# Performance work log

Measured on AMD Instinct MI355X. Metric: run time of the kernel, lower is better.

Reference implementation:

```python
import jax, jax.numpy as jnp
import numpy as np

N_NODES = 50000
N_EDGES = 800000
IN_F = 128
HID = 64
OUT_F = 64
H = 1  # num_heads


def _gat_layer(x, W, al, ar, b, src, dst, n_nodes):
    # DGL GATConv: project, per-head attention logits, edge softmax over dst, scatter-sum
    h, f = al.shape
    feat = (x @ W).reshape(x.shape[0], h, f)              # [N,H,F]
    el = jnp.sum(feat * al, axis=-1)                       # [N,H]
    er = jnp.sum(feat * ar, axis=-1)                       # [N,H]
    e = jax.nn.leaky_relu(el[src] + er[dst], negative_slope=0.2)  # [E,H]
    emax = jax.ops.segment_max(e, dst, num_segments=n_nodes)      # [N,H]
    ex = jnp.exp(e - emax[dst])                            # [E,H]
    denom = jax.ops.segment_sum(ex, dst, num_segments=n_nodes)    # [N,H]
    alpha = ex / denom[dst]                                # [E,H] edge softmax
    msg = feat[src] * alpha[:, :, None]                    # [E,H,F]
    out = jax.ops.segment_sum(msg, dst, num_segments=n_nodes) + b # [N,H,F]
    return out


def setup_inputs() -> dict:
    key = jax.random.key(0)
    ks = jax.random.split(key, 20)

    def glorot(k, shape, fan_in):
        return jax.random.normal(k, shape, dtype=jnp.float32) / np.sqrt(fan_in)

    x = jax.random.normal(ks[0], (N_NODES, IN_F), dtype=jnp.float32)
    src = jax.random.randint(ks[1], (N_EDGES,), 0, N_NODES, dtype=jnp.int32)
    dst = jax.random.randint(ks[2], (N_EDGES,), 0, N_NODES, dtype=jnp.int32)
    neg_src = jax.random.randint(ks[3], (N_EDGES,), 0, N_NODES, dtype=jnp.int32)
    neg_dst = jax.random.randint(ks[4], (N_EDGES,), 0, N_NODES, dtype=jnp.int32)

    # layer dims: 128 -> 64 -> 128 -> 64 (hidden, hidden*2, out), H=1, mean over heads
    W1 = glorot(ks[5], (IN_F, H * HID), IN_F)
    al1 = glorot(ks[6], (H, HID), HID)
    ar1 = glorot(ks[7], (H, HID), HID)
    b1 = jnp.zeros((H, HID), dtype=jnp.float32)
    W2 = glorot(ks[8], (HID, H * 2 * HID), HID)
    al2 = glorot(ks[9], (H, 2 * HID), 2 * HID)
    ar2 = glorot(ks[10], (H, 2 * HID), 2 * HID)
    b2 = jnp.zeros((H, 2 * HID), dtype=jnp.float32)
    W3 = glorot(ks[11], (2 * HID, H * OUT_F), 2 * HID)
    al3 = glorot(ks[12], (H, OUT_F), OUT_F)
    ar3 = glorot(ks[13], (H, OUT_F), OUT_F)
    b3 = jnp.zeros((H, OUT_F), dtype=jnp.float32)
    lp_W = glorot(ks[14], (2 * OUT_F, 1), 2 * OUT_F)
    lp_b = jnp.zeros((1,), dtype=jnp.float32)

    return {
        "x": x, "W1": W1, "al1": al1, "ar1": ar1, "b1": b1,
        "W2": W2, "al2": al2, "ar2": ar2, "b2": b2,
        "W3": W3, "al3": al3, "ar3": ar3, "b3": b3,
        "lp_W": lp_W, "lp_b": lp_b,
        "src": src, "dst": dst, "neg_src": neg_src, "neg_dst": neg_dst,
    }


def reference(x, W1, al1, ar1, b1, W2, al2, ar2, b2, W3, al3, ar3, b3,
              lp_W, lp_b, src, dst, neg_src, neg_dst):
    n = x.shape[0]
    h = jax.nn.relu(_gat_layer(x, W1, al1, ar1, b1, src, dst, n)).mean(axis=1)
    h = jax.nn.relu(_gat_layer(h, W2, al2, ar2, b2, src, dst, n)).mean(axis=1)
    h = _gat_layer(h, W3, al3, ar3, b3, src, dst, n).mean(axis=1)      # [N,OUT_F]
    pos_score = (jnp.concatenate([h[src], h[dst]], axis=1) @ lp_W + lp_b)[:, 0]
    neg_score = (jnp.concatenate([h[neg_src], h[neg_dst]], axis=1) @ lp_W + lp_b)[:, 0]
    return h, pos_score, neg_score
```

## Files before the change

kernel.cpp:

```cpp
#include <hip/hip_runtime.h>
#include <hip/hip_bf16.h>

#define NN 50000
#define NE 800000
#define NBKT 196
#define NT 200
#define TILE 4000

typedef unsigned short ushort_t;
typedef unsigned int uint_t;

typedef __bf16 bf16_t;
typedef bf16_t bf16x8 __attribute__((ext_vector_type(8)));
typedef float f32x4 __attribute__((ext_vector_type(4)));

__device__ __forceinline__ float leaky(float v) { return (v >= 0.f) ? v : 0.2f * v; }
__device__ __forceinline__ ushort_t f2bf(float f) {
    __hip_bfloat16 h = __float2bfloat16(f);
    return *reinterpret_cast<ushort_t*>(&h);
}
__device__ __forceinline__ float bf_lo(uint_t v) { return __uint_as_float(v << 16); }
__device__ __forceinline__ float bf_hi(uint_t v) { return __uint_as_float(v & 0xFFFF0000u); }


#define WELEM (128 * 64 * 3)
#define WBLK 96

__global__ void prep_hist(const float* __restrict__ W1, const float* __restrict__ W2,
                          const float* __restrict__ W3, ushort_t* __restrict__ Wt1,
                          ushort_t* __restrict__ Wt2, ushort_t* __restrict__ Wt3,
                          const float* __restrict__ al2, const float* __restrict__ ar2,
                          float* __restrict__ val2, float* __restrict__ var2,
                          const int* __restrict__ dst, uint_t* __restrict__ gh) {
    __shared__ uint_t h[NBKT];
    int tid = threadIdx.x;
    int blk = blockIdx.x;
    if (blk < NT) {
        for (int i = tid; i < NBKT; i += 256) h[i] = 0;
        __syncthreads();
        int e0 = blk * TILE;
        for (int i = tid; i < TILE; i += 256)
            atomicAdd(&h[((uint_t)dst[e0 + i]) >> 8], 1u);
        __syncthreads();
        for (int i = tid; i < NBKT; i += 256) gh[(size_t)i * NT + blk] = h[i];
        return;
    }
    blk -= NT;
    if (blk < WBLK) {
        int gw = blk * 256 + tid;
        if (gw < 128 * 64) {
            int i = gw; int k = i >> 6, m = i & 63;
            Wt1[m * 128 + k] = f2bf(W1[i]);
        } else if (gw < 2 * 128 * 64) {
            int i = gw - 128 * 64; int k = i >> 7, m = i & 127;
            Wt2[m * 64 + k] = f2bf(W2[i]);
        } else if (gw < WELEM) {
            int i = gw - 2 * 128 * 64; int k = i >> 6, m = i & 63;
            Wt3[m * 128 + k] = f2bf(W3[i]);
        }
        return;
    }
    if (tid < 128) {
        int k = tid & 63;
        const float* av = (tid < 64) ? al2 : ar2;
        float acc = 0.f;
        const float* row = W2 + k * 128;
        #pragma unroll 8
        for (int m = 0; m < 128; ++m) acc += row[m] * av[m];
        if (tid < 64) val2[k] = acc; else var2[k] = acc;
    }
}

__global__ void scan_gh(uint_t* __restrict__ gh, uint_t* __restrict__ bucketbase) {
    __shared__ uint_t btot[NBKT];
    __shared__ uint_t ws4[4];
    int tid = threadIdx.x;
    int wv = tid >> 6, lane = tid & 63;
    for (int b = wv; b < NBKT; b += 16) {
        uint_t* row = gh + (size_t)b * NT;
        uint_t carry = 0;
        for (int base = 0; base < NT; base += 64) {
            int idx = base + lane;
            uint_t v = (idx < NT) ? row[idx] : 0;
            uint_t sc = v;
            for (int o = 1; o < 64; o <<= 1) {
                uint_t xx = __shfl_up(sc, o);
                if (lane >= o) sc += xx;
            }
            if (idx < NT) row[idx] = carry + sc - v;
            carry += __shfl(sc, 63);
        }
        if (lane == 0) btot[b] = carry;
    }
    __syncthreads();
    uint_t v = 0, sc = 0;
    if (tid < 256) {
        v = (tid < NBKT) ? btot[tid] : 0;
        sc = v;
        for (int o = 1; o < 64; o <<= 1) {
            uint_t xx = __shfl_up(sc, o);
            if ((tid & 63) >= o) sc += xx;
        }
        if ((tid & 63) == 63) ws4[tid >> 6] = sc;
    }
    __syncthreads();
    if (tid == 0) {
        uint_t r = 0;
        for (int i = 0; i < 4; ++i) { uint_t tmp = ws4[i]; ws4[i] = r; r += tmp; }
    }
    __syncthreads();
    if (tid < NBKT) bucketbase[tid] = ws4[tid >> 6] + sc - v;
    if (tid == 0) bucketbase[NBKT] = NE;
}

__global__ void part_scatter(const int* __restrict__ src, const int* __restrict__ dst,
                             const uint_t* __restrict__ gh, const uint_t* __restrict__ bucketbase,
                             uint_t* __restrict__ pairbuf) {
    __shared__ uint_t cur[NBKT];
    int t = blockIdx.x, tid = threadIdx.x;
    for (int i = tid; i < NBKT; i += 256)
        cur[i] = gh[(size_t)i * NT + t] + bucketbase[i];
    __syncthreads();
    int e0 = t * TILE;
    for (int i = tid; i < TILE; i += 256) {
        int d = dst[e0 + i], s = src[e0 + i];
        uint_t pos = atomicAdd(&cur[((uint_t)d) >> 8], 1u);
        pairbuf[pos] = (uint_t)s | (((uint_t)d & 255u) << 16);
    }
}

__device__ __forceinline__ void gemm64_f32core(const float* __restrict__ X,
                                               const ushort_t* __restrict__ Wt,
                                               const float* __restrict__ al,
                                               const float* __restrict__ ar,
                                               ushort_t* __restrict__ featbf,
                                               float* __restrict__ el, float* __restrict__ er,
                                               int N, int blk, int tid) {
    constexpr int CT = 4, KI = 4;
    int wv = tid >> 6, lane = tid & 63;
    int c = lane & 15, kq = lane >> 4;
    int n0 = blk * 64 + wv * 16;
    if (n0 >= N) return;

    const float* aptr = X + (size_t)(n0 + c) * 128 + kq * 8;
    bf16x8 a[KI];
    #pragma unroll
    for (int ki = 0; ki < KI; ++ki) {
        float4 f0 = *reinterpret_cast<const float4*>(aptr + ki * 32);
        float4 f1 = *reinterpret_cast<const float4*>(aptr + ki * 32 + 4);
        union { bf16x8 v; ushort_t u[8]; } pk;
        pk.u[0] = f2bf(f0.x); pk.u[1] = f2bf(f0.y); pk.u[2] = f2bf(f0.z); pk.u[3] = f2bf(f0.w);
        pk.u[4] = f2bf(f1.x); pk.u[5] = f2bf(f1.y); pk.u[6] = f2bf(f1.z); pk.u[7] = f2bf(f1.w);
        a[ki] = pk.v;
    }

    f32x4 acc[CT];
    #pragma unroll
    for (int ct = 0; ct < CT; ++ct) acc[ct] = (f32x4){0.f, 0.f, 0.f, 0.f};

    #pragma unroll
    for (int ct = 0; ct < CT; ++ct) {
        const ushort_t* bptr = Wt + (size_t)(ct * 16 + c) * 128 + kq * 8;
        #pragma unroll
        for (int ki = 0; ki < KI; ++ki) {
            bf16x8 b = *reinterpret_cast<const bf16x8*>(bptr + ki * 32);
            acc[ct] = __builtin_amdgcn_mfma_f32_16x16x32_bf16(a[ki], b, acc[ct], 0, 0, 0);
        }
    }

    float pe[4] = {0.f, 0.f, 0.f, 0.f}, pr[4] = {0.f, 0.f, 0.f, 0.f};
    #pragma unroll
    for (int ct = 0; ct < CT; ++ct) {
        float alv = al[ct * 16 + c], arv = ar[ct * 16 + c];
        #pragma unroll
        for (int j = 0; j < 4; ++j) {
            float v = acc[ct][j];
            featbf[(size_t)(n0 + kq * 4 + j) * 64 + ct * 16 + c] = f2bf(v);
            pe[j] += v * alv;
            pr[j] += v * arv;
        }
    }
    #pragma unroll
    for (int o = 1; o < 16; o <<= 1) {
        #pragma unroll
        for (int j = 0; j < 4; ++j) {
            pe[j] += __shfl_xor(pe[j], o);
            pr[j] += __shfl_xor(pr[j], o);
        }
    }
    if (c == 0) {
        #pragma unroll
        for (int j = 0; j < 4; ++j) {
            el[n0 + kq * 4 + j] = pe[j];
            er[n0 + kq * 4 + j] = pr[j];
        }
    }
}

__global__ void csr_gemm1(const uint_t* __restrict__ pairbuf, const uint_t* __restrict__ bucketbase,
                          int* __restrict__ off, int* __restrict__ csrsrc,
                          const float* __restrict__ X, const ushort_t* __restrict__ Wt1,
                          const float* __restrict__ al1, const float* __restrict__ ar1,
                          ushort_t* __restrict__ featbf, float* __restrict__ el,
                          float* __restrict__ er, int N) {
    __shared__ uint_t cnt[256];
    __shared__ uint_t ws4[4];
    int tid = threadIdx.x;
    if (blockIdx.x >= NBKT) {
        gemm64_f32core(X, Wt1, al1, ar1, featbf, el, er, N, blockIdx.x - NBKT, tid);
        return;
    }
    int b = blockIdx.x;
    uint_t eb0 = bucketbase[b], m = bucketbase[b + 1] - eb0;
    cnt[tid] = 0;
    __syncthreads();
    for (uint_t i = tid; i < m; i += 256)
        atomicAdd(&cnt[pairbuf[eb0 + i] >> 16], 1u);
    __syncthreads();
    uint_t v = cnt[tid];
    int lane = tid & 63, w = tid >> 6;
    uint_t sc = v;
    for (int o = 1; o < 64; o <<= 1) {
        uint_t x = __shfl_up(sc, o);
        if (lane >= o) sc += x;
    }
    if (lane == 63) ws4[w] = sc;
    __syncthreads();
    if (tid == 0) { uint_t r = 0; for (int i = 0; i < 4; ++i) { uint_t tmp = ws4[i]; ws4[i] = r; r += tmp; } }
    __syncthreads();
    uint_t excl = ws4[w] + sc - v;
    int node = b * 256 + tid;
    if (node < NN) off[node] = (int)(eb0 + excl);
    if (b == 0 && tid == 0) off[NN] = NE;
    __syncthreads();
    cnt[tid] = eb0 + excl;
    __syncthreads();
    for (uint_t i = tid; i < m; i += 256) {
        uint_t p = pairbuf[eb0 + i];
        uint_t pos = atomicAdd(&cnt[p >> 16], 1u);
        csrsrc[pos] = (int)(p & 0xFFFFu);
    }
}

__global__ void fused_l23(const ushort_t* __restrict__ G, const ushort_t* __restrict__ Wt2,
                          const float* __restrict__ b2, const ushort_t* __restrict__ Wt3,
                          const float* __restrict__ al3, const float* __restrict__ ar3,
                          ushort_t* __restrict__ feat3, float* __restrict__ el,
                          float* __restrict__ er, int N) {
    __shared__ ushort_t h3s[4][16 * 128];
    int wv = threadIdx.x >> 6, lane = threadIdx.x & 63;
    int c = lane & 15, kq = lane >> 4;
    int n0 = blockIdx.x * 64 + wv * 16;
    if (n0 >= N) return;

    const ushort_t* aptr = G + (size_t)(n0 + c) * 64 + kq * 8;
    bf16x8 a1[2];
    a1[0] = *reinterpret_cast<const bf16x8*>(aptr);
    a1[1] = *reinterpret_cast<const bf16x8*>(aptr + 32);

    f32x4 acc2[8];
    #pragma unroll
    for (int ct = 0; ct < 8; ++ct) acc2[ct] = (f32x4){0.f, 0.f, 0.f, 0.f};
    #pragma unroll
    for (int ct = 0; ct < 8; ++ct) {
        const ushort_t* bptr = Wt2 + (size_t)(ct * 16 + c) * 64 + kq * 8;
        acc2[ct] = __builtin_amdgcn_mfma_f32_16x16x32_bf16(
            a1[0], *reinterpret_cast<const bf16x8*>(bptr), acc2[ct], 0, 0, 0);
        acc2[ct] = __builtin_amdgcn_mfma_f32_16x16x32_bf16(
            a1[1], *reinterpret_cast<const bf16x8*>(bptr + 32), acc2[ct], 0, 0, 0);
    }

    #pragma unroll
    for (int ct = 0; ct < 8; ++ct) {
        float bv = b2[ct * 16 + c];
        #pragma unroll
        for (int j = 0; j < 4; ++j) {
            int r = kq * 4 + j;
            float v = fmaxf(acc2[ct][j] + bv, 0.f);
            h3s[wv][r * 128 + ((ct * 16 + c) ^ ((r & 7) << 3))] = f2bf(v);
        }
    }

    bf16x8 a2[4];
    #pragma unroll
    for (int ki = 0; ki < 4; ++ki)
        a2[ki] = *reinterpret_cast<const bf16x8*>(
            &h3s[wv][c * 128 + ((ki * 32 + kq * 8) ^ ((c & 7) << 3))]);

    f32x4 acc3[4];
    #pragma unroll
    for (int ct = 0; ct < 4; ++ct) acc3[ct] = (f32x4){0.f, 0.f, 0.f, 0.f};
    #pragma unroll
    for (int ct = 0; ct < 4; ++ct) {
        const ushort_t* bptr = Wt3 + (size_t)(ct * 16 + c) * 128 + kq * 8;
        #pragma unroll
        for (int ki = 0; ki < 4; ++ki) {
            bf16x8 b = *reinterpret_cast<const bf16x8*>(bptr + ki * 32);
            acc3[ct] = __builtin_amdgcn_mfma_f32_16x16x32_bf16(a2[ki], b, acc3[ct], 0, 0, 0);
        }
    }

    float pe[4] = {0.f, 0.f, 0.f, 0.f}, pr[4] = {0.f, 0.f, 0.f, 0.f};
    #pragma unroll
    for (int ct = 0; ct < 4; ++ct) {
        float alv = al3[ct * 16 + c], arv = ar3[ct * 16 + c];
        #pragma unroll
        for (int j = 0; j < 4; ++j) {
            float v = acc3[ct][j];
            feat3[(size_t)(n0 + kq * 4 + j) * 64 + ct * 16 + c] = f2bf(v);
            pe[j] += v * alv;
            pr[j] += v * arv;
        }
    }
    #pragma unroll
    for (int o = 1; o < 16; o <<= 1) {
        #pragma unroll
        for (int j = 0; j < 4; ++j) {
            pe[j] += __shfl_xor(pe[j], o);
            pr[j] += __shfl_xor(pr[j], o);
        }
    }
    if (c == 0) {
        #pragma unroll
        for (int j = 0; j < 4; ++j) {
            el[n0 + kq * 4 + j] = pe[j];
            er[n0 + kq * 4 + j] = pr[j];
        }
    }
}

template <bool BIAS, bool RELU, bool BFOUT, bool DOTS>
__global__ void gat_agg2(const int* __restrict__ off, const int* __restrict__ csrsrc,
                         const float* __restrict__ el, const float* __restrict__ er,
                         const ushort_t* __restrict__ featbf, const float* __restrict__ bias,
                         void* __restrict__ hout, const float* __restrict__ va,
                         const float* __restrict__ vb, float* __restrict__ o1,
                         float* __restrict__ o2, int N) {
    int g = blockIdx.x * blockDim.x + threadIdx.x;
    int node = g >> 5;
    int sub = threadIdx.x & 31;
    if (node >= N) return;
    int start = off[node], deg = off[node + 1] - start;
    float ern = er[node];

    int s0 = 0; float e0 = -1e30f;
    if (sub < deg) { s0 = csrsrc[start + sub]; e0 = leaky(el[s0] + ern); }
    float m = e0;
    for (int i = 32 + sub; i < deg; i += 32)
        m = fmaxf(m, leaky(el[csrsrc[start + i]] + ern));
    for (int o = 16; o; o >>= 1) m = fmaxf(m, __shfl_xor(m, o));

    float p0 = (sub < deg) ? __expf(e0 - m) : 0.f;
    float ssum = p0;
    for (int i = 32 + sub; i < deg; i += 32)
        ssum += __expf(leaky(el[csrsrc[start + i]] + ern) - m);
    for (int o = 16; o; o >>= 1) ssum += __shfl_xor(ssum, o);
    float inv = (deg > 0) ? 1.f / ssum : 0.f;

    float acc0 = 0.f, acc1 = 0.f;
    int head = (deg < 32) ? deg : 32;
    int i = 0;
    for (; i + 4 <= head; i += 4) {
        float pA = __shfl(p0, i, 32), pB = __shfl(p0, i + 1, 32),
              pC = __shfl(p0, i + 2, 32), pD = __shfl(p0, i + 3, 32);
        int sA = __shfl(s0, i, 32), sB = __shfl(s0, i + 1, 32),
            sC = __shfl(s0, i + 2, 32), sD = __shfl(s0, i + 3, 32);
        uint_t vA = ((const uint_t*)(featbf + (size_t)sA * 64))[sub];
        uint_t vB = ((const uint_t*)(featbf + (size_t)sB * 64))[sub];
        uint_t vC = ((const uint_t*)(featbf + (size_t)sC * 64))[sub];
        uint_t vD = ((const uint_t*)(featbf + (size_t)sD * 64))[sub];
        acc0 += pA * bf_lo(vA) + pB * bf_lo(vB) + pC * bf_lo(vC) + pD * bf_lo(vD);
        acc1 += pA * bf_hi(vA) + pB * bf_hi(vB) + pC * bf_hi(vC) + pD * bf_hi(vD);
    }
    for (; i < head; ++i) {
        float p = __shfl(p0, i, 32);
        int sN = __shfl(s0, i, 32);
        uint_t v = ((const uint_t*)(featbf + (size_t)sN * 64))[sub];
        acc0 += p * bf_lo(v); acc1 += p * bf_hi(v);
    }
    for (i = 32; i < deg; ++i) {
        int sN = csrsrc[start + i];
        float p = __expf(leaky(el[sN] + ern) - m);
        uint_t v = ((const uint_t*)(featbf + (size_t)sN * 64))[sub];
        acc0 += p * bf_lo(v); acc1 += p * bf_hi(v);
    }

    float v0 = acc0 * inv, v1 = acc1 * inv;
    if (BIAS) {
        float2 b2 = ((const float2*)bias)[sub];
        v0 += b2.x; v1 += b2.y;
    }
    if (RELU) { v0 = fmaxf(v0, 0.f); v1 = fmaxf(v1, 0.f); }
    if (BFOUT) {
        ((uint_t*)hout)[(size_t)node * 32 + sub] = ((uint_t)f2bf(v1) << 16) | f2bf(v0);
    } else {
        ((float2*)hout)[(size_t)node * 32 + sub] = make_float2(v0, v1);
    }
    if (DOTS) {
        float2 wa = ((const float2*)va)[sub];
        float2 wb = ((const float2*)vb)[sub];
        float a = v0 * wa.x + v1 * wa.y;
        float b = v0 * wb.x + v1 * wb.y;
        for (int o = 16; o; o >>= 1) { a += __shfl_xor(a, o); b += __shfl_xor(b, o); }
        if (sub == 0) { o1[node] = a; o2[node] = b; }
    }
}

__global__ void scores4_k(const int4* __restrict__ s4, const int4* __restrict__ d4,
                          const int4* __restrict__ ns4, const int4* __restrict__ nd4,
                          const float* __restrict__ s1, const float* __restrict__ s2,
                          const float* __restrict__ lpb,
                          float4* __restrict__ outp, float4* __restrict__ outn, int E4) {
    int i = blockIdx.x * blockDim.x + threadIdx.x;
    float cc = lpb[0];
    if (i < E4) {
        int4 s = s4[i], d = d4[i];
        outp[i] = make_float4(s1[s.x] + s2[d.x] + cc, s1[s.y] + s2[d.y] + cc,
                              s1[s.z] + s2[d.z] + cc, s1[s.w] + s2[d.w] + cc);
    } else if (i < 2 * E4) {
        int j = i - E4;
        int4 s = ns4[j], d = nd4[j];
        outn[j] = make_float4(s1[s.x] + s2[d.x] + cc, s1[s.y] + s2[d.y] + cc,
                              s1[s.z] + s2[d.z] + cc, s1[s.w] + s2[d.w] + cc);
    }
}


struct Scratch {
    ushort_t* wt1; ushort_t* wt2; ushort_t* wt3;
    ushort_t* featbf; ushort_t* hAbf;
    float* elA; float* erA; float* elB; float* erB;
    float* val2; float* var2; float* s1; float* s2;
    int* off; int* csrsrc; uint_t* gh; uint_t* bucketbase;
    uint_t* pairbuf;
};

extern "C" void kernel_launch(void* const* d_in, const int* in_sizes, int n_in,
                              void* d_out, int out_size, void* d_ws, size_t ws_size,
                              hipStream_t stream) {
    const float* x   = (const float*)d_in[0];
    const float* W1  = (const float*)d_in[1];
    const float* al1 = (const float*)d_in[2];
    const float* ar1 = (const float*)d_in[3];
    const float* b1  = (const float*)d_in[4];
    const float* W2  = (const float*)d_in[5];
    const float* al2 = (const float*)d_in[6];
    const float* ar2 = (const float*)d_in[7];
    const float* b2  = (const float*)d_in[8];
    const float* W3  = (const float*)d_in[9];
    const float* al3 = (const float*)d_in[10];
    const float* ar3 = (const float*)d_in[11];
    const float* b3  = (const float*)d_in[12];
    const float* lpW = (const float*)d_in[13];
    const float* lpb = (const float*)d_in[14];
    const int* src  = (const int*)d_in[15];
    const int* dst  = (const int*)d_in[16];
    const int* nsrc = (const int*)d_in[17];
    const int* ndst = (const int*)d_in[18];

    char* w = (char*)d_ws;
    Scratch S;
    S.featbf     = (ushort_t*)w; w += (size_t)NN * 64 * 2;
    S.hAbf       = (ushort_t*)w; w += (size_t)NN * 64 * 2;
    S.wt1        = (ushort_t*)w; w += 128 * 64 * 2;
    S.wt2        = (ushort_t*)w; w += 64 * 128 * 2;
    S.wt3        = (ushort_t*)w; w += 128 * 64 * 2;
    S.elA        = (float*)w;    w += (size_t)NN * 4;
    S.erA        = (float*)w;    w += (size_t)NN * 4;
    S.elB        = (float*)w;    w += (size_t)NN * 4;
    S.erB        = (float*)w;    w += (size_t)NN * 4;
    S.val2       = (float*)w;    w += 64 * 4;
    S.var2       = (float*)w;    w += 64 * 4;
    S.s1         = (float*)w;    w += (size_t)NN * 4;
    S.s2         = (float*)w;    w += (size_t)NN * 4;
    S.off        = (int*)w;      w += (size_t)(NN + 1) * 4;
    S.csrsrc     = (int*)w;      w += (size_t)NE * 4;
    S.gh         = (uint_t*)w;   w += (size_t)NBKT * NT * 4;
    S.bucketbase = (uint_t*)w;   w += (size_t)(NBKT + 1) * 4;
    S.pairbuf    = (uint_t*)w;   w += (size_t)NE * 4;

    const int GEMM_GRID = (NN + 63) / 64;
    const int AGG_GRID = (NN * 32 + 255) / 256;

    prep_hist<<<NT + WBLK + 1, 256, 0, stream>>>(
        W1, W2, W3, S.wt1, S.wt2, S.wt3, al2, ar2, S.val2, S.var2, dst, S.gh);
    scan_gh<<<1, 1024, 0, stream>>>(S.gh, S.bucketbase);
    part_scatter<<<NT, 256, 0, stream>>>(src, dst, S.gh, S.bucketbase, S.pairbuf);
    csr_gemm1<<<NBKT + GEMM_GRID, 256, 0, stream>>>(
        S.pairbuf, S.bucketbase, S.off, S.csrsrc,
        x, S.wt1, al1, ar1, S.featbf, S.elA, S.erA, NN);

    float* out_h   = (float*)d_out;
    float* out_pos = out_h + (size_t)NN * 64;
    float* out_neg = out_pos + NE;

    gat_agg2<true, true, true, true><<<AGG_GRID, 256, 0, stream>>>(
        S.off, S.csrsrc, S.elA, S.erA, S.featbf, b1, S.hAbf,
        S.val2, S.var2, S.elB, S.erB, NN);
    gat_agg2<false, false, true, false><<<AGG_GRID, 256, 0, stream>>>(
        S.off, S.csrsrc, S.elB, S.erB, S.hAbf, nullptr, S.featbf,
        nullptr, nullptr, nullptr, nullptr, NN);
    fused_l23<<<GEMM_GRID, 256, 0, stream>>>(S.featbf, S.wt2, b2, S.wt3, al3, ar3,
                                             S.hAbf, S.elA, S.erA, NN);
    gat_agg2<true, false, false, true><<<AGG_GRID, 256, 0, stream>>>(
        S.off, S.csrsrc, S.elA, S.erA, S.hAbf, b3, out_h,
        lpW, lpW + 64, S.s1, S.s2, NN);
    const int E4 = NE / 4;
    scores4_k<<<(2 * E4 + 255) / 256, 256, 0, stream>>>(
        (const int4*)src, (const int4*)dst, (const int4*)nsrc, (const int4*)ndst,
        S.s1, S.s2, lpb, (float4*)out_pos, (float4*)out_neg, E4);
}
```

Baseline: 164.0 us.

## Store layer-1 and layer-2 gathered features as int8 with per-row scales

Layer-1 projected features and layer-1 aggregation output are now quantized to int8 with a per-node absmax scale instead of bf16. The scale is folded into the softmax weight during the gather. This halves the bytes moved by the random per-edge feature gathers in the first two aggregation passes. In exchange it loses precision, which may exceed tolerance, and adds a warp reduction for the scale plus an extra scale load per edge.

```diff
diff --git a/kernel.cpp b/kernel.cpp
--- a/kernel.cpp
+++ b/kernel.cpp
@@ -9,6 +9,7 @@
 
 typedef unsigned short ushort_t;
 typedef unsigned int uint_t;
+typedef signed char s8_t;
 
 typedef __bf16 bf16_t;
 typedef bf16_t bf16x8 __attribute__((ext_vector_type(8)));
@@ -133,7 +134,8 @@
                                                const ushort_t* __restrict__ Wt,
                                                const float* __restrict__ al,
                                                const float* __restrict__ ar,
-                                               ushort_t* __restrict__ featbf,
+                                               s8_t* __restrict__ feat8,
+                                               float* __restrict__ scl,
                                                float* __restrict__ el, float* __restrict__ er,
                                                int N, int blk, int tid) {
     constexpr int CT = 4, KI = 4;
@@ -169,15 +171,16 @@
     }
 
     float pe[4] = {0.f, 0.f, 0.f, 0.f}, pr[4] = {0.f, 0.f, 0.f, 0.f};
+    float pm[4] = {0.f, 0.f, 0.f, 0.f};
     #pragma unroll
     for (int ct = 0; ct < CT; ++ct) {
         float alv = al[ct * 16 + c], arv = ar[ct * 16 + c];
         #pragma unroll
         for (int j = 0; j < 4; ++j) {
             float v = acc[ct][j];
-            featbf[(size_t)(n0 + kq * 4 + j) * 64 + ct * 16 + c] = f2bf(v);
             pe[j] += v * alv;
             pr[j] += v * arv;
+            pm[j] = fmaxf(pm[j], fabsf(v));
         }
     }
     #pragma unroll
@@ -186,6 +189,17 @@
         for (int j = 0; j < 4; ++j) {
             pe[j] += __shfl_xor(pe[j], o);
             pr[j] += __shfl_xor(pr[j], o);
+            pm[j] = fmaxf(pm[j], __shfl_xor(pm[j], o));
+        }
+    }
+    #pragma unroll
+    for (int j = 0; j < 4; ++j) {
+        float qi = (pm[j] > 0.f) ? 127.f / pm[j] : 0.f;
+        int row = n0 + kq * 4 + j;
+        #pragma unroll
+        for (int ct = 0; ct < CT; ++ct) {
+            int q = (int)rintf(acc[ct][j] * qi);
+            feat8[(size_t)row * 64 + ct * 16 + c] = (s8_t)q;
         }
     }
     if (c == 0) {
@@ -193,6 +207,7 @@
         for (int j = 0; j < 4; ++j) {
             el[n0 + kq * 4 + j] = pe[j];
             er[n0 + kq * 4 + j] = pr[j];
+            scl[n0 + kq * 4 + j] = pm[j] * (1.f / 127.f);
         }
     }
 }
@@ -201,13 +216,13 @@
                           int* __restrict__ off, int* __restrict__ csrsrc,
                           const float* __restrict__ X, const ushort_t* __restrict__ Wt1,
                           const float* __restrict__ al1, const float* __restrict__ ar1,
-                          ushort_t* __restrict__ featbf, float* __restrict__ el,
-                          float* __restrict__ er, int N) {
+                          s8_t* __restrict__ feat8, float* __restrict__ scl1,
+                          float* __restrict__ el, float* __restrict__ er, int N) {
     __shared__ uint_t cnt[256];
     __shared__ uint_t ws4[4];
     int tid = threadIdx.x;
     if (blockIdx.x >= NBKT) {
-        gemm64_f32core(X, Wt1, al1, ar1, featbf, el, er, N, blockIdx.x - NBKT, tid);
+        gemm64_f32core(X, Wt1, al1, ar1, feat8, scl1, el, er, N, blockIdx.x - NBKT, tid);
         return;
     }
     int b = blockIdx.x;
@@ -329,11 +344,12 @@
     }
 }
 
-template <bool BIAS, bool RELU, bool BFOUT, bool DOTS>
+template <int INFMT, int OUTFMT, bool BIAS, bool RELU, bool DOTS>
 __global__ void gat_agg2(const int* __restrict__ off, const int* __restrict__ csrsrc,
                          const float* __restrict__ el, const float* __restrict__ er,
-                         const ushort_t* __restrict__ featbf, const float* __restrict__ bias,
-                         void* __restrict__ hout, const float* __restrict__ va,
+                         const void* __restrict__ featv, const float* __restrict__ inscl,
+                         const float* __restrict__ bias, void* __restrict__ hout,
+                         float* __restrict__ outscl, const float* __restrict__ va,
                          const float* __restrict__ vb, float* __restrict__ o1,
                          float* __restrict__ o2, int N) {
     int g = blockIdx.x * blockDim.x + threadIdx.x;
@@ -343,8 +359,12 @@
     int start = off[node], deg = off[node + 1] - start;
     float ern = er[node];
 
-    int s0 = 0; float e0 = -1e30f;
-    if (sub < deg) { s0 = csrsrc[start + sub]; e0 = leaky(el[s0] + ern); }
+    int s0 = 0; float e0 = -1e30f; float sc0 = 0.f;
+    if (sub < deg) {
+        s0 = csrsrc[start + sub];
+        e0 = leaky(el[s0] + ern);
+        if (INFMT == 0) sc0 = inscl[s0];
+    }
     float m = e0;
     for (int i = 32 + sub; i < deg; i += 32)
         m = fmaxf(m, leaky(el[csrsrc[start + i]] + ern));
@@ -357,32 +377,60 @@
     for (int o = 16; o; o >>= 1) ssum += __shfl_xor(ssum, o);
     float inv = (deg > 0) ? 1.f / ssum : 0.f;
 
+    float ps0 = (INFMT == 0) ? p0 * sc0 : p0;
+
     float acc0 = 0.f, acc1 = 0.f;
     int head = (deg < 32) ? deg : 32;
     int i = 0;
     for (; i + 4 <= head; i += 4) {
-        float pA = __shfl(p0, i, 32), pB = __shfl(p0, i + 1, 32),
-              pC = __shfl(p0, i + 2, 32), pD = __shfl(p0, i + 3, 32);
+        float pA = __shfl(ps0, i, 32), pB = __shfl(ps0, i + 1, 32),
+              pC = __shfl(ps0, i + 2, 32), pD = __shfl(ps0, i + 3, 32);
         int sA = __shfl(s0, i, 32), sB = __shfl(s0, i + 1, 32),
             sC = __shfl(s0, i + 2, 32), sD = __shfl(s0, i + 3, 32);
-        uint_t vA = ((const uint_t*)(featbf + (size_t)sA * 64))[sub];
-        uint_t vB = ((const uint_t*)(featbf + (size_t)sB * 64))[sub];
-        uint_t vC = ((const uint_t*)(featbf + (size_t)sC * 64))[sub];
-        uint_t vD = ((const uint_t*)(featbf + (size_t)sD * 64))[sub];
-        acc0 += pA * bf_lo(vA) + pB * bf_lo(vB) + pC * bf_lo(vC) + pD * bf_lo(vD);
-        acc1 += pA * bf_hi(vA) + pB * bf_hi(vB) + pC * bf_hi(vC) + pD * bf_hi(vD);
+        if (INFMT == 0) {
+            const s8_t* base = (const s8_t*)featv;
+            ushort_t uA = ((const ushort_t*)(base + (size_t)sA * 64))[sub];
+            ushort_t uB = ((const ushort_t*)(base + (size_t)sB * 64))[sub];
+            ushort_t uC = ((const ushort_t*)(base + (size_t)sC * 64))[sub];
+            ushort_t uD = ((const ushort_t*)(base + (size_t)sD * 64))[sub];
+            acc0 += pA * (float)(s8_t)(uA & 0xFF) + pB * (float)(s8_t)(uB & 0xFF)
+                  + pC * (float)(s8_t)(uC & 0xFF) + pD * (float)(s8_t)(uD & 0xFF);
+            acc1 += pA * (float)(s8_t)(uA >> 8) + pB * (float)(s8_t)(uB >> 8)
+                  + pC * (float)(s8_t)(uC >> 8) + pD * (float)(s8_t)(uD >> 8);
+        } else {
+            const ushort_t* base = (const ushort_t*)featv;
+            uint_t vA = ((const uint_t*)(base + (size_t)sA * 64))[sub];
+            uint_t vB = ((const uint_t*)(base + (size_t)sB * 64))[sub];
+            uint_t vC = ((const uint_t*)(base + (size_t)sC * 64))[sub];
+            uint_t vD = ((const uint_t*)(base + (size_t)sD * 64))[sub];
+            acc0 += pA * bf_lo(vA) + pB * bf_lo(vB) + pC * bf_lo(vC) + pD * bf_lo(vD);
+            acc1 += pA * bf_hi(vA) + pB * bf_hi(vB) + pC * bf_hi(vC) + pD * bf_hi(vD);
+        }
     }
     for (; i < head; ++i) {
-        float p = __shfl(p0, i, 32);
+        float p = __shfl(ps0, i, 32);
         int sN = __shfl(s0, i, 32);
-        uint_t v = ((const uint_t*)(featbf + (size_t)sN * 64))[sub];
-        acc0 += p * bf_lo(v); acc1 += p * bf_hi(v);
+        if (INFMT == 0) {
+            ushort_t u = ((const ushort_t*)((const s8_t*)featv + (size_t)sN * 64))[sub];
+            acc0 += p * (float)(s8_t)(u & 0xFF);
+            acc1 += p * (float)(s8_t)(u >> 8);
+        } else {
+            uint_t v = ((const uint_t*)((const ushort_t*)featv + (size_t)sN * 64))[sub];
+            acc0 += p * bf_lo(v); acc1 += p * bf_hi(v);
+        }
     }
     for (i = 32; i < deg; ++i) {
         int sN = csrsrc[start + i];
         float p = __expf(leaky(el[sN] + ern) - m);
-        uint_t v = ((const uint_t*)(featbf + (size_t)sN * 64))[sub];
-        acc0 += p * bf_lo(v); acc1 += p * bf_hi(v);
+        if (INFMT == 0) {
+            p *= inscl[sN];
+            ushort_t u = ((const ushort_t*)((const s8_t*)featv + (size_t)sN * 64))[sub];
+            acc0 += p * (float)(s8_t)(u & 0xFF);
+            acc1 += p * (float)(s8_t)(u >> 8);
+        } else {
+            uint_t v = ((const uint_t*)((const ushort_t*)featv + (size_t)sN * 64))[sub];
+            acc0 += p * bf_lo(v); acc1 += p * bf_hi(v);
+        }
     }
 
     float v0 = acc0 * inv, v1 = acc1 * inv;
@@ -391,11 +439,21 @@
         v0 += b2.x; v1 += b2.y;
     }
     if (RELU) { v0 = fmaxf(v0, 0.f); v1 = fmaxf(v1, 0.f); }
-    if (BFOUT) {
+
+    if (OUTFMT == 0) {
+        float rm = fmaxf(fabsf(v0), fabsf(v1));
+        for (int o = 16; o; o >>= 1) rm = fmaxf(rm, __shfl_xor(rm, o));
+        float qi = (rm > 0.f) ? 127.f / rm : 0.f;
+        int q0 = (int)rintf(v0 * qi), q1 = (int)rintf(v1 * qi);
+        ((ushort_t*)hout)[(size_t)node * 32 + sub] =
+            (ushort_t)((q0 & 0xFF) | ((q1 & 0xFF) << 8));
+        if (sub == 0) outscl[node] = rm * (1.f / 127.f);
+    } else if (OUTFMT == 1) {
         ((uint_t*)hout)[(size_t)node * 32 + sub] = ((uint_t)f2bf(v1) << 16) | f2bf(v0);
     } else {
         ((float2*)hout)[(size_t)node * 32 + sub] = make_float2(v0, v1);
     }
+
     if (DOTS) {
         float2 wa = ((const float2*)va)[sub];
         float2 wb = ((const float2*)vb)[sub];
@@ -428,7 +486,9 @@
 
 struct Scratch {
     ushort_t* wt1; ushort_t* wt2; ushort_t* wt3;
-    ushort_t* featbf; ushort_t* hAbf;
+    s8_t* feat8; float* scl1;
+    s8_t* hA8; float* sclA;
+    ushort_t* gbf; ushort_t* f3bf;
     float* elA; float* erA; float* elB; float* erB;
     float* val2; float* var2; float* s1; float* s2;
     int* off; int* csrsrc; uint_t* gh; uint_t* bucketbase;
@@ -460,8 +520,12 @@
 
     char* w = (char*)d_ws;
     Scratch S;
-    S.featbf     = (ushort_t*)w; w += (size_t)NN * 64 * 2;
-    S.hAbf       = (ushort_t*)w; w += (size_t)NN * 64 * 2;
+    S.feat8      = (s8_t*)w;     w += (size_t)NN * 64;
+    S.hA8        = (s8_t*)w;     w += (size_t)NN * 64;
+    S.gbf        = (ushort_t*)w; w += (size_t)NN * 64 * 2;
+    S.f3bf       = (ushort_t*)w; w += (size_t)NN * 64 * 2;
+    S.scl1       = (float*)w;    w += (size_t)NN * 4;
+    S.sclA       = (float*)w;    w += (size_t)NN * 4;
     S.wt1        = (ushort_t*)w; w += 128 * 64 * 2;
     S.wt2        = (ushort_t*)w; w += 64 * 128 * 2;
     S.wt3        = (ushort_t*)w; w += 128 * 64 * 2;
@@ -488,22 +552,22 @@
     part_scatter<<<NT, 256, 0, stream>>>(src, dst, S.gh, S.bucketbase, S.pairbuf);
     csr_gemm1<<<NBKT + GEMM_GRID, 256, 0, stream>>>(
         S.pairbuf, S.bucketbase, S.off, S.csrsrc,
-        x, S.wt1, al1, ar1, S.featbf, S.elA, S.erA, NN);
+        x, S.wt1, al1, ar1, S.feat8, S.scl1, S.elA, S.erA, NN);
 
     float* out_h   = (float*)d_out;
     float* out_pos = out_h + (size_t)NN * 64;
     float* out_neg = out_pos + NE;
 
-    gat_agg2<true, true, true, true><<<AGG_GRID, 256, 0, stream>>>(
-        S.off, S.csrsrc, S.elA, S.erA, S.featbf, b1, S.hAbf,
+    gat_agg2<0, 0, true, true, true><<<AGG_GRID, 256, 0, stream>>>(
+        S.off, S.csrsrc, S.elA, S.erA, S.feat8, S.scl1, b1, S.hA8, S.sclA,
         S.val2, S.var2, S.elB, S.erB, NN);
-    gat_agg2<false, false, true, false><<<AGG_GRID, 256, 0, stream>>>(
-        S.off, S.csrsrc, S.elB, S.erB, S.hAbf, nullptr, S.featbf,
+    gat_agg2<0, 1, false, false, false><<<AGG_GRID, 256, 0, stream>>>(
+        S.off, S.csrsrc, S.elB, S.erB, S.hA8, S.sclA, nullptr, S.gbf, nullptr,
         nullptr, nullptr, nullptr, nullptr, NN);
-    fused_l23<<<GEMM_GRID, 256, 0, stream>>>(S.featbf, S.wt2, b2, S.wt3, al3, ar3,
-                                             S.hAbf, S.elA, S.erA, NN);
-    gat_agg2<true, false, false, true><<<AGG_GRID, 256, 0, stream>>>(
-        S.off, S.csrsrc, S.elA, S.erA, S.hAbf, b3, out_h,
+    fused_l23<<<GEMM_GRID, 256, 0, stream>>>(S.gbf, S.wt2, b2, S.wt3, al3, ar3,
+                                             S.f3bf, S.elA, S.erA, NN);
+    gat_agg2<1, 2, true, false, true><<<AGG_GRID, 256, 0, stream>>>(
+        S.off, S.csrsrc, S.elA, S.erA, S.f3bf, nullptr, b3, out_h, nullptr,
         lpW, lpW + 64, S.s1, S.s2, NN);
     const int E4 = NE / 4;
     scores4_k<<<(2 * E4 + 255) / 256, 256, 0, stream>>>(
```

Result: no change. 162.0 us (-1.2%).
